# Kernel tuning notes

Measured on AMD Instinct MI355X. Metric: run time of the kernel, lower is better.

## Reference

```python
import jax, jax.numpy as jnp
import numpy as np

H = 1024      # hidden_dim
NH = 16       # num_heads
HD = H // NH  # head_dim
FFN = 4096
EPS = 1e-5


def setup_inputs() -> dict:
    key = jax.random.key(0)
    ks = jax.random.split(key, 12)
    s = 0.02
    return {
        "x": jax.random.normal(ks[0], (2, 2048, H), dtype=jnp.float32),
        "w_qkv": jax.random.normal(ks[1], (H, 3 * H), dtype=jnp.float32) * s,
        "b_qkv": jnp.zeros((3 * H,), dtype=jnp.float32),
        "w_out": jax.random.normal(ks[2], (H, H), dtype=jnp.float32) * s,
        "b_out": jnp.zeros((H,), dtype=jnp.float32),
        "ln1_g": jnp.ones((H,), dtype=jnp.float32),
        "ln1_b": jnp.zeros((H,), dtype=jnp.float32),
        "ln2_g": jnp.ones((H,), dtype=jnp.float32),
        "ln2_b": jnp.zeros((H,), dtype=jnp.float32),
        "w1": jax.random.normal(ks[3], (H, FFN), dtype=jnp.float32) * s,
        "b1": jnp.zeros((FFN,), dtype=jnp.float32),
        "w2": jax.random.normal(ks[4], (FFN, H), dtype=jnp.float32) * s,
        "b2": jnp.zeros((H,), dtype=jnp.float32),
    }


def _layernorm(x, g, b):
    mu = jnp.mean(x, axis=-1, keepdims=True)
    var = jnp.mean(jnp.square(x - mu), axis=-1, keepdims=True)
    return (x - mu) * jax.lax.rsqrt(var + EPS) * g + b


def reference(x, w_qkv, b_qkv, w_out, b_out, ln1_g, ln1_b, ln2_g, ln2_b, w1, b1, w2, b2):
    B, S, _ = x.shape
    # pre-LN attention branch
    h = _layernorm(x, ln1_g, ln1_b)
    qkv = h @ w_qkv + b_qkv                       # (B,S,3H)
    qkv = qkv.reshape(B, S, 3, NH, HD).transpose(2, 0, 3, 1, 4)
    q, k, v = qkv[0], qkv[1], qkv[2]              # (B,NH,S,HD)
    scores = jnp.einsum("bhqd,bhkd->bhqk", q, k) / jnp.sqrt(jnp.float32(HD))
    causal = jnp.triu(jnp.ones((S, S), dtype=bool), k=1)
    scores = jnp.where(causal, -jnp.inf, scores)
    attn = jax.nn.softmax(scores, axis=-1)
    out = jnp.einsum("bhqk,bhkd->bhqd", attn, v)  # (B,NH,S,HD)
    out = out.transpose(0, 2, 1, 3).reshape(B, S, H)
    attn_out = out @ w_out + b_out
    x = x + attn_out
    # FFN branch
    h2 = _layernorm(x, ln2_g, ln2_b)
    ffn = jax.nn.gelu(h2 @ w1 + b1, approximate=False) @ w2 + b2
    return x + ffn
```

## Files before the change

kernel.cpp:

```cpp
#include <hip/hip_runtime.h>
#include <hip/hip_bf16.h>

typedef __bf16 bf16_t;
typedef __bf16 bf16x8 __attribute__((ext_vector_type(8)));
typedef __bf16 bf16x4 __attribute__((ext_vector_type(4)));
typedef __bf16 bf16x2 __attribute__((ext_vector_type(2)));
typedef float  f32x4  __attribute__((ext_vector_type(4)));

#define HDIM 1024
#define SEQ  2048
#define NHEAD 16
#define HEADD 64

__device__ __forceinline__ void gld_lds16(const void* g, void* l) {
  __builtin_amdgcn_global_load_lds(
      (const __attribute__((address_space(1))) unsigned int*)g,
      (__attribute__((address_space(3))) unsigned int*)l, 16, 0, 0);
}

__global__ __launch_bounds__(256) void ln_kernel(const float* __restrict__ x,
                                                 const float* __restrict__ gam,
                                                 const float* __restrict__ bet,
                                                 bf16_t* __restrict__ out) {
  int row = blockIdx.x;
  int t = threadIdx.x;
  const float4* xr = (const float4*)(x + (size_t)row * HDIM);
  float4 v = xr[t];
  float s = v.x + v.y + v.z + v.w;
  float ss = v.x*v.x + v.y*v.y + v.z*v.z + v.w*v.w;
  #pragma unroll
  for (int o = 32; o > 0; o >>= 1) {
    s  += __shfl_xor(s, o);
    ss += __shfl_xor(ss, o);
  }
  __shared__ float red[8];
  int w = t >> 6;
  if ((t & 63) == 0) { red[w*2] = s; red[w*2+1] = ss; }
  __syncthreads();
  s  = red[0] + red[2] + red[4] + red[6];
  ss = red[1] + red[3] + red[5] + red[7];
  float mu  = s * (1.0f / HDIM);
  float var = ss * (1.0f / HDIM) - mu * mu;
  float rstd = rsqrtf(var + 1e-5f);
  float4 g4 = ((const float4*)gam)[t];
  float4 b4 = ((const float4*)bet)[t];
  bf16x4 o4;
  o4[0] = (bf16_t)((v.x - mu) * rstd * g4.x + b4.x);
  o4[1] = (bf16_t)((v.y - mu) * rstd * g4.y + b4.y);
  o4[2] = (bf16_t)((v.z - mu) * rstd * g4.z + b4.z);
  o4[3] = (bf16_t)((v.w - mu) * rstd * g4.w + b4.w);
  *(bf16x4*)(out + (size_t)row * HDIM + t * 4) = o4;
}

__global__ __launch_bounds__(256) void transpose_cast(const float* __restrict__ W,
                                                      bf16_t* __restrict__ Wt,
                                                      int Kd, int Nd) {
  __shared__ float tile[32][33];
  int n0 = blockIdx.x * 32, k0 = blockIdx.y * 32;
  int tx = threadIdx.x & 31, ty = threadIdx.x >> 5;
  #pragma unroll
  for (int i = 0; i < 4; i++)
    tile[ty + i*8][tx] = W[(size_t)(k0 + ty + i*8) * Nd + n0 + tx];
  __syncthreads();
  #pragma unroll
  for (int i = 0; i < 4; i++)
    Wt[(size_t)(n0 + ty + i*8) * Kd + k0 + tx] = (bf16_t)tile[tx][ty + i*8];
}

__device__ __forceinline__ float gelu_fast(float x) {
  float y = 0.7978845608f * (x + 0.044715f * x * x * x);
  float u = exp2f(y * 2.885390082f);
  float th = 1.0f - 2.0f * __builtin_amdgcn_rcpf(u + 1.0f);
  return 0.5f * x * (1.0f + th);
}

template<int EPI, int BN>
__global__ __launch_bounds__(256, 2)
void gemm_bt(const bf16_t* __restrict__ A, const bf16_t* __restrict__ Bt,
             const float* __restrict__ bias, const float* __restrict__ resid,
             void* __restrict__ outp, int M, int N, int K) {
  constexpr int NFRAG = BN / 32;
  __shared__ bf16_t As[2][128*32];
  __shared__ bf16_t Bs[2][BN*32];
  int t = threadIdx.x;
  int w = t >> 6, l = t & 63;
  int wr = w >> 1, wc = w & 1;

  int nbx = gridDim.x;
  int bid = blockIdx.y * nbx + blockIdx.x;
  int chunk = (nbx * gridDim.y) >> 3;
  int nb = (bid & 7) * chunk + (bid >> 3);
  int bm = nb / nbx, bn = nb % nbx;
  size_t m0 = (size_t)bm * 128, n0 = (size_t)bn * BN;

  f32x4 acc[4][NFRAG];
  #pragma unroll
  for (int m = 0; m < 4; m++)
    #pragma unroll
    for (int n = 0; n < NFRAG; n++) acc[m][n] = (f32x4)(0.0f);

  int srow = t >> 2, scol = (t & 3) * 8;
  int soff = srow * 32 + scol;
  const bf16_t* ag = A  + (m0 + srow) * K + scol;
  const bf16_t* bg = Bt + (n0 + srow) * K + scol;

  int lr = l & 15, lc = (l >> 4) * 8;

  auto stage = [&](int buf, int k0) {
    gld_lds16(ag + k0, &As[buf][soff]);
    gld_lds16(ag + k0 + (size_t)64 * K, &As[buf][soff + 64*32]);
    gld_lds16(bg + k0, &Bs[buf][soff]);
    if constexpr (BN == 128)
      gld_lds16(bg + k0 + (size_t)64 * K, &Bs[buf][soff + 64*32]);
  };

  stage(0, 0);
  __syncthreads();
  int cur = 0;
  for (int k0 = 0; k0 < K; k0 += 32) {
    if (k0 + 32 < K) stage(cur ^ 1, k0 + 32);
    bf16x8 af[4], bfr[NFRAG];
    #pragma unroll
    for (int m = 0; m < 4; m++)
      af[m] = *(const bf16x8*)(&As[cur][(wr*64 + m*16 + lr)*32 + lc]);
    #pragma unroll
    for (int n = 0; n < NFRAG; n++)
      bfr[n] = *(const bf16x8*)(&Bs[cur][(wc*(BN/2) + n*16 + lr)*32 + lc]);
    #pragma unroll
    for (int m = 0; m < 4; m++)
      #pragma unroll
      for (int n = 0; n < NFRAG; n++)
        acc[m][n] = __builtin_amdgcn_mfma_f32_16x16x32_bf16(af[m], bfr[n], acc[m][n], 0, 0, 0);
    __syncthreads();
    cur ^= 1;
  }

  int r0 = (l >> 4) * 4, c0 = l & 15;
  #pragma unroll
  for (int m = 0; m < 4; m++) {
    #pragma unroll
    for (int n = 0; n < NFRAG; n++) {
      size_t row = m0 + wr*64 + m*16 + r0;
      size_t col = n0 + wc*(BN/2) + n*16 + c0;
      float bv = bias[col];
      #pragma unroll
      for (int r = 0; r < 4; r++) {
        float vv = acc[m][n][r] + bv;
        size_t idx = (row + r) * (size_t)N + col;
        if (EPI == 0) {
          ((bf16_t*)outp)[idx] = (bf16_t)vv;
        } else if (EPI == 1) {
          ((float*)outp)[idx] = vv + resid[idx];
        } else {
          ((bf16_t*)outp)[idx] = (bf16_t)gelu_fast(vv);
        }
      }
    }
  }
}

__global__ __launch_bounds__(512, 4)
void attn_kernel(const bf16_t* __restrict__ qkv, bf16_t* __restrict__ out) {
  int idx = blockIdx.x;
  int half = idx >> 8;
  int sub = idx & 255;
  int qth = sub >> 5;
  int qt = half ? qth : (15 - qth);
  int bh = sub & 31;
  int b = bh >> 4, h = bh & 15;
  int t = threadIdx.x, w = t >> 6, l = t & 63;

  __shared__ bf16_t Ks[2][64*64];
  __shared__ bf16_t Vt[2][64*72];
  __shared__ bf16_t Ps[8][16*64];

  const size_t RS = 3 * HDIM;
  const bf16_t* qb = qkv + (size_t)b * SEQ * RS + h * HEADD;
  const bf16_t* kb = qb + HDIM;
  const bf16_t* vb = qb + 2 * HDIM;

  int lr = l & 15, lg = l >> 4;
  const float SCALE = 0.125f * 1.44269504f;

  bf16x8 qf[2];
  {
    size_t qrow = (size_t)qt * 128 + w * 16 + lr;
    qf[0] = *(const bf16x8*)(qb + qrow * RS + lg * 8);
    qf[1] = *(const bf16x8*)(qb + qrow * RS + 32 + lg * 8);
    #pragma unroll
    for (int i = 0; i < 8; i++) {
      qf[0][i] = (bf16_t)((float)qf[0][i] * SCALE);
      qf[1][i] = (bf16_t)((float)qf[1][i] * SCALE);
    }
  }

  f32x4 o[4];
  #pragma unroll
  for (int d = 0; d < 4; d++) o[d] = (f32x4)(0.0f);
  float m = -1e30f, lsum = 0.0f;

  int srow = t >> 3, scol = (t & 7) * 8;
  int Fv = ((scol >> 3) & 7) << 3;
  int nkt = 2 * qt + 2;

  const bf16_t* kg0 = kb + (size_t)srow * RS + scol;
  const bf16_t* vg0 = vb + (size_t)srow * RS + scol;

  bf16x8 kr = *(const bf16x8*)kg0;
  bf16x8 vr = *(const bf16x8*)vg0;

  int wrow0 = qt * 128 + w * 16;
  int qg = wrow0 + lr;
  bf16_t* pw = Ps[w];
  int psw = (lr & 7) << 4;
  int cur = 0;

  for (int kt = 0; kt < nkt; kt++) {
    {
      int ba = srow * 128 + scol * 2;
      int sw = (srow & 7) << 4;
      *(bf16x8*)((char*)Ks[cur] + (ba ^ sw)) = kr;
      int ksw = srow ^ Fv;
      bf16_t* vt = Vt[cur];
      #pragma unroll
      for (int i = 0; i < 8; i++)
        vt[(scol + i) * 72 + ksw] = vr[i];
    }
    if (kt + 1 < nkt) {
      kr = *(const bf16x8*)(kg0 + (size_t)(kt + 1) * 64 * RS);
      vr = *(const bf16x8*)(vg0 + (size_t)(kt + 1) * 64 * RS);
    }
    __syncthreads();

    bool skipw = (kt * 64) > (wrow0 + 15);
    if (!skipw) {
      f32x4 sc[4];
      #pragma unroll
      for (int kt2 = 0; kt2 < 4; kt2++) {
        sc[kt2] = (f32x4)(0.0f);
        #pragma unroll
        for (int kk = 0; kk < 2; kk++) {
          int row = kt2 * 16 + lr;
          int off = (row * 128 + kk * 64 + lg * 16) ^ ((row & 7) << 4);
          bf16x8 kf = *(const bf16x8*)((char*)Ks[cur] + off);
          sc[kt2] = __builtin_amdgcn_mfma_f32_16x16x32_bf16(kf, qf[kk], sc[kt2], 0, 0, 0);
        }
      }
      if (kt * 64 + 63 > wrow0) {
        #pragma unroll
        for (int kt2 = 0; kt2 < 4; kt2++) {
          #pragma unroll
          for (int r = 0; r < 4; r++) {
            int kcol = kt*64 + kt2*16 + lg*4 + r;
            if (kcol > qg) sc[kt2][r] = -1e30f;
          }
        }
      }
      float tm0 = fmaxf(fmaxf(sc[0][0], sc[0][1]), fmaxf(sc[0][2], sc[0][3]));
      float tm1 = fmaxf(fmaxf(sc[1][0], sc[1][1]), fmaxf(sc[1][2], sc[1][3]));
      float tm2 = fmaxf(fmaxf(sc[2][0], sc[2][1]), fmaxf(sc[2][2], sc[2][3]));
      float tm3 = fmaxf(fmaxf(sc[3][0], sc[3][1]), fmaxf(sc[3][2], sc[3][3]));
      float tm = fmaxf(fmaxf(tm0, tm1), fmaxf(tm2, tm3));
      tm = fmaxf(tm, __shfl_xor(tm, 16));
      tm = fmaxf(tm, __shfl_xor(tm, 32));
      if (!__all(tm <= m + 8.0f)) {
        float nm = fmaxf(m, tm);
        float alpha = exp2f(m - nm);
        m = nm;
        lsum *= alpha;
        #pragma unroll
        for (int d = 0; d < 4; d++)
          #pragma unroll
          for (int r = 0; r < 4; r++) o[d][r] *= alpha;
      }
      #pragma unroll
      for (int kt2 = 0; kt2 < 4; kt2++) {
        float p0 = exp2f(sc[kt2][0] - m);
        float p1 = exp2f(sc[kt2][1] - m);
        float p2 = exp2f(sc[kt2][2] - m);
        float p3 = exp2f(sc[kt2][3] - m);
        lsum += (p0 + p1) + (p2 + p3);
        bf16x2 pa; pa[0] = (bf16_t)p0; pa[1] = (bf16_t)p1;
        bf16x2 pb; pb[0] = (bf16_t)p2; pb[1] = (bf16_t)p3;
        int base = lr * 128 + kt2 * 32 + lg * 8;
        *(bf16x2*)((char*)pw + ((base)     ^ psw)) = pa;
        *(bf16x2*)((char*)pw + ((base + 4) ^ psw)) = pb;
      }
      asm volatile("s_waitcnt lgkmcnt(0)" ::: "memory");
      #pragma unroll
      for (int kk = 0; kk < 2; kk++) {
        int poff = (lr * 128 + kk * 64 + lg * 16) ^ psw;
        bf16x8 pf = *(const bf16x8*)((char*)pw + poff);
        #pragma unroll
        for (int dblk = 0; dblk < 4; dblk++) {
          int vrow = dblk * 16 + lr;
          int Fd = ((vrow >> 3) & 7) << 3;
          bf16x8 vf = *(const bf16x8*)(Vt[cur] + vrow * 72 + ((kk * 32 + lg * 8) ^ Fd));
          o[dblk] = __builtin_amdgcn_mfma_f32_16x16x32_bf16(vf, pf, o[dblk], 0, 0, 0);
        }
      }
    }
    cur ^= 1;
  }

  lsum += __shfl_xor(lsum, 16);
  lsum += __shfl_xor(lsum, 32);
  float inv = 1.0f / lsum;

  bf16_t* ob = out + ((size_t)b * SEQ + qg) * HDIM + h * HEADD;
  #pragma unroll
  for (int dblk = 0; dblk < 4; dblk++) {
    bf16x4 q4;
    #pragma unroll
    for (int r = 0; r < 4; r++) q4[r] = (bf16_t)(o[dblk][r] * inv);
    *(bf16x4*)(ob + dblk * 16 + lg * 4) = q4;
  }
}

extern "C" void kernel_launch(void* const* d_in, const int* in_sizes, int n_in,
                              void* d_out, int out_size, void* d_ws, size_t ws_size,
                              hipStream_t stream) {
  (void)in_sizes; (void)n_in; (void)out_size; (void)ws_size;
  const float* x     = (const float*)d_in[0];
  const float* w_qkv = (const float*)d_in[1];
  const float* b_qkv = (const float*)d_in[2];
  const float* w_out = (const float*)d_in[3];
  const float* b_out = (const float*)d_in[4];
  const float* ln1_g = (const float*)d_in[5];
  const float* ln1_b = (const float*)d_in[6];
  const float* ln2_g = (const float*)d_in[7];
  const float* ln2_b = (const float*)d_in[8];
  const float* w1    = (const float*)d_in[9];
  const float* b1    = (const float*)d_in[10];
  const float* w2    = (const float*)d_in[11];
  const float* b2    = (const float*)d_in[12];
  float* out = (float*)d_out;

  char* ws = (char*)d_ws;
  size_t off = 0;
  auto alloc = [&](size_t bytes) -> void* {
    void* p = ws + off;
    off += (bytes + 255) & ~(size_t)255;
    return p;
  };
  bf16_t* wqkvT = (bf16_t*)alloc((size_t)3072*1024*2);
  bf16_t* woutT = (bf16_t*)alloc((size_t)1024*1024*2);
  bf16_t* w1T   = (bf16_t*)alloc((size_t)4096*1024*2);
  bf16_t* w2T   = (bf16_t*)alloc((size_t)1024*4096*2);
  bf16_t* ln1o  = (bf16_t*)alloc((size_t)4096*1024*2);
  bf16_t* qkvb  = (bf16_t*)alloc((size_t)4096*4096*2);
  bf16_t* attno = (bf16_t*)alloc((size_t)4096*1024*2);
  float*  x2    = (float*) alloc((size_t)4096*1024*4);
  bf16_t* h2 = ln1o;
  bf16_t* g  = qkvb;

  dim3 blk(256);
  transpose_cast<<<dim3(3072/32, 1024/32), blk, 0, stream>>>(w_qkv, wqkvT, 1024, 3072);
  transpose_cast<<<dim3(1024/32, 1024/32), blk, 0, stream>>>(w_out, woutT, 1024, 1024);
  transpose_cast<<<dim3(4096/32, 1024/32), blk, 0, stream>>>(w1,    w1T,   1024, 4096);
  transpose_cast<<<dim3(1024/32, 4096/32), blk, 0, stream>>>(w2,    w2T,   4096, 1024);

  ln_kernel<<<4096, blk, 0, stream>>>(x, ln1_g, ln1_b, ln1o);
  gemm_bt<0,128><<<dim3(24, 32), blk, 0, stream>>>(ln1o, wqkvT, b_qkv, nullptr, qkvb, 4096, 3072, 1024);
  attn_kernel<<<512, dim3(512), 0, stream>>>(qkvb, attno);
  gemm_bt<1,64><<<dim3(16, 32), blk, 0, stream>>>(attno, woutT, b_out, x, x2, 4096, 1024, 1024);
  ln_kernel<<<4096, blk, 0, stream>>>(x2, ln2_g, ln2_b, h2);
  gemm_bt<2,128><<<dim3(32, 32), blk, 0, stream>>>(h2, w1T, b1, nullptr, g, 4096, 4096, 1024);
  gemm_bt<1,64><<<dim3(16, 32), blk, 0, stream>>>(g, w2T, b2, x2, out, 4096, 1024, 4096);
}
```

Before: 252.6 us.

## Parametrize GEMM K-tile depth and add XOR-swizzled LDS layout

The GEMM kernel gains a BK template parameter. Staging now uses an XOR swizzle on the 16-byte chunk index so that fragment reads from LDS avoid bank conflicts. The two N=1024 GEMMs (out-projection and FFN down) switch to BK=64, which halves the number of k-iterations and barriers per tile at the cost of doubled LDS per block. The BK=32 instances also pick up the swizzle, which changes their LDS access pattern.

New measurement: 236.1 us. 6.5% less time.

```diff
diff --git a/kernel.cpp b/kernel.cpp
--- a/kernel.cpp
+++ b/kernel.cpp
@@ -74,22 +74,25 @@
   return 0.5f * x * (1.0f + th);
 }
 
-template<int EPI, int BN>
+template<int EPI, int BN, int BK>
 __global__ __launch_bounds__(256, 2)
 void gemm_bt(const bf16_t* __restrict__ A, const bf16_t* __restrict__ Bt,
              const float* __restrict__ bias, const float* __restrict__ resid,
              void* __restrict__ outp, int M, int N, int K) {
   constexpr int NFRAG = BN / 32;
-  __shared__ bf16_t As[2][128*32];
-  __shared__ bf16_t Bs[2][BN*32];
+  constexpr int CH  = BK / 8;
+  constexpr int SWZ = CH - 1;
+  constexpr int RPP = 256 / CH;
+  __shared__ bf16_t As[2][128*BK];
+  __shared__ bf16_t Bs[2][BN*BK];
   int t = threadIdx.x;
   int w = t >> 6, l = t & 63;
   int wr = w >> 1, wc = w & 1;
 
   int nbx = gridDim.x;
   int bid = blockIdx.y * nbx + blockIdx.x;
-  int chunk = (nbx * gridDim.y) >> 3;
-  int nb = (bid & 7) * chunk + (bid >> 3);
+  int chunkx = (nbx * gridDim.y) >> 3;
+  int nb = (bid & 7) * chunkx + (bid >> 3);
   int bm = nb / nbx, bn = nb % nbx;
   size_t m0 = (size_t)bm * 128, n0 = (size_t)bn * BN;
 
@@ -99,38 +102,49 @@
     #pragma unroll
     for (int n = 0; n < NFRAG; n++) acc[m][n] = (f32x4)(0.0f);
 
-  int srow = t >> 2, scol = (t & 3) * 8;
-  int soff = srow * 32 + scol;
+  int srow = t / CH;
+  int scol = ((t & SWZ) ^ (srow & SWZ)) * 8;
+  int dsto = t * 8;
   const bf16_t* ag = A  + (m0 + srow) * K + scol;
   const bf16_t* bg = Bt + (n0 + srow) * K + scol;
 
-  int lr = l & 15, lc = (l >> 4) * 8;
+  int lr = l & 15, lg = l >> 4;
 
   auto stage = [&](int buf, int k0) {
-    gld_lds16(ag + k0, &As[buf][soff]);
-    gld_lds16(ag + k0 + (size_t)64 * K, &As[buf][soff + 64*32]);
-    gld_lds16(bg + k0, &Bs[buf][soff]);
-    if constexpr (BN == 128)
-      gld_lds16(bg + k0 + (size_t)64 * K, &Bs[buf][soff + 64*32]);
+    #pragma unroll
+    for (int p = 0; p < 128/RPP; p++)
+      gld_lds16(ag + k0 + (size_t)(p*RPP)*K, &As[buf][dsto + p*RPP*BK]);
+    #pragma unroll
+    for (int p = 0; p < BN/RPP; p++)
+      gld_lds16(bg + k0 + (size_t)(p*RPP)*K, &Bs[buf][dsto + p*RPP*BK]);
   };
 
   stage(0, 0);
   __syncthreads();
   int cur = 0;
-  for (int k0 = 0; k0 < K; k0 += 32) {
-    if (k0 + 32 < K) stage(cur ^ 1, k0 + 32);
-    bf16x8 af[4], bfr[NFRAG];
-    #pragma unroll
-    for (int m = 0; m < 4; m++)
-      af[m] = *(const bf16x8*)(&As[cur][(wr*64 + m*16 + lr)*32 + lc]);
-    #pragma unroll
-    for (int n = 0; n < NFRAG; n++)
-      bfr[n] = *(const bf16x8*)(&Bs[cur][(wc*(BN/2) + n*16 + lr)*32 + lc]);
-    #pragma unroll
-    for (int m = 0; m < 4; m++)
-      #pragma unroll
-      for (int n = 0; n < NFRAG; n++)
-        acc[m][n] = __builtin_amdgcn_mfma_f32_16x16x32_bf16(af[m], bfr[n], acc[m][n], 0, 0, 0);
+  for (int k0 = 0; k0 < K; k0 += BK) {
+    if (k0 + BK < K) stage(cur ^ 1, k0 + BK);
+    #pragma unroll
+    for (int kk = 0; kk < BK/32; kk++) {
+      bf16x8 af[4], bfr[NFRAG];
+      #pragma unroll
+      for (int m = 0; m < 4; m++) {
+        int row = wr*64 + m*16 + lr;
+        int off = row*BK*2 + (((kk*4 + lg) ^ (row & SWZ)) << 4);
+        af[m] = *(const bf16x8*)((const char*)&As[cur][0] + off);
+      }
+      #pragma unroll
+      for (int n = 0; n < NFRAG; n++) {
+        int row = wc*(BN/2) + n*16 + lr;
+        int off = row*BK*2 + (((kk*4 + lg) ^ (row & SWZ)) << 4);
+        bfr[n] = *(const bf16x8*)((const char*)&Bs[cur][0] + off);
+      }
+      #pragma unroll
+      for (int m = 0; m < 4; m++)
+        #pragma unroll
+        for (int n = 0; n < NFRAG; n++)
+          acc[m][n] = __builtin_amdgcn_mfma_f32_16x16x32_bf16(af[m], bfr[n], acc[m][n], 0, 0, 0);
+    }
     __syncthreads();
     cur ^= 1;
   }
@@ -361,10 +375,10 @@
   transpose_cast<<<dim3(1024/32, 4096/32), blk, 0, stream>>>(w2,    w2T,   4096, 1024);
 
   ln_kernel<<<4096, blk, 0, stream>>>(x, ln1_g, ln1_b, ln1o);
-  gemm_bt<0,128><<<dim3(24, 32), blk, 0, stream>>>(ln1o, wqkvT, b_qkv, nullptr, qkvb, 4096, 3072, 1024);
+  gemm_bt<0,128,32><<<dim3(24, 32), blk, 0, stream>>>(ln1o, wqkvT, b_qkv, nullptr, qkvb, 4096, 3072, 1024);
   attn_kernel<<<512, dim3(512), 0, stream>>>(qkvb, attno);
-  gemm_bt<1,64><<<dim3(16, 32), blk, 0, stream>>>(attno, woutT, b_out, x, x2, 4096, 1024, 1024);
+  gemm_bt<1,64,64><<<dim3(16, 32), blk, 0, stream>>>(attno, woutT, b_out, x, x2, 4096, 1024, 1024);
   ln_kernel<<<4096, blk, 0, stream>>>(x2, ln2_g, ln2_b, h2);
-  gemm_bt<2,128><<<dim3(32, 32), blk, 0, stream>>>(h2, w1T, b1, nullptr, g, 4096, 4096, 1024);
-  gemm_bt<1,64><<<dim3(16, 32), blk, 0, stream>>>(g, w2T, b2, x2, out, 4096, 1024, 4096);
-}
+  gemm_bt<2,128,32><<<dim3(32, 32), blk, 0, stream>>>(h2, w1T, b1, nullptr, g, 4096, 4096, 1024);
+  gemm_bt<1,64,64><<<dim3(16, 32), blk, 0, stream>>>(g, w2T, b2, x2, out, 4096, 1024, 4096);
+}
```
